# Performance work log

Hardware: AMD Instinct MI355X
Metric: run time of the kernel (lower is better)

## Reference

```python
import jax, jax.numpy as jnp
import numpy as np

N_HEADS, D_MODEL, D_HEAD = 16, 1024, 64
LN_EPS = 1e-5


def setup_inputs() -> dict:
    key = jax.random.key(0)
    ks = jax.random.split(key, 12)
    bs, s = 2, 2048
    hd = N_HEADS * D_HEAD
    sc = 0.02
    return {
        "q": jax.random.normal(ks[0], (bs, s, D_MODEL), jnp.float32),
        "kv": jax.random.normal(ks[1], (bs, s, D_MODEL), jnp.float32),
        "Wq": jax.random.normal(ks[2], (D_MODEL, hd), jnp.float32) * sc,
        "bq": jnp.zeros((hd,), jnp.float32),
        "Wk": jax.random.normal(ks[3], (D_MODEL, hd), jnp.float32) * sc,
        "bk": jnp.zeros((hd,), jnp.float32),
        "Wv": jax.random.normal(ks[4], (D_MODEL, hd), jnp.float32) * sc,
        "bv": jnp.zeros((hd,), jnp.float32),
        "Wo": jax.random.normal(ks[5], (hd, D_MODEL), jnp.float32) * sc,
        "bo": jnp.zeros((D_MODEL,), jnp.float32),
        "gamma": jnp.ones((D_MODEL,), jnp.float32),
        "beta": jnp.zeros((D_MODEL,), jnp.float32),
    }


def _split_heads(x):
    # [b, s, H*D] -> [b, H, s, D]
    b, s, _ = x.shape
    return x.reshape(b, s, N_HEADS, D_HEAD).transpose(0, 2, 1, 3)


def reference(q, kv, Wq, bq, Wk, bk, Wv, bv, Wo, bo, gamma, beta):
    wq = _split_heads(q @ Wq + bq)   # [b,H,Sq,D]
    wk = _split_heads(kv @ Wk + bk)  # [b,H,Sk,D]
    wv = _split_heads(kv @ Wv + bv)  # [b,H,Sk,D]
    scores = jnp.einsum("bhqd,bhkd->bhqk", wq, wk) / jnp.sqrt(
        jnp.asarray(D_HEAD, wq.dtype)
    )
    probs = jax.nn.softmax(scores, axis=-1)  # dropout p=0 -> identity
    attn = jnp.einsum("bhqk,bhkd->bhqd", probs, wv)
    b, _, sq, _ = attn.shape
    attn = attn.transpose(0, 2, 1, 3).reshape(b, sq, N_HEADS * D_HEAD)
    res = q + (attn @ Wo + bo)
    # LayerNorm over last dim
    mu = jnp.mean(res, axis=-1, keepdims=True)
    var = jnp.var(res, axis=-1, keepdims=True)
    return (res - mu) * jax.lax.rsqrt(var + LN_EPS) * gamma + beta
```

## Files before the change

kernel.cpp:

```cpp
#include <hip/hip_runtime.h>
#include <hip/hip_bf16.h>


#define DM 1024
#define SEQ 2048
#define NB 2
#define NH 16
#define DH 64

typedef __attribute__((ext_vector_type(8))) short bf16x8;
typedef __attribute__((ext_vector_type(4))) float f32x4;
typedef __attribute__((ext_vector_type(4))) unsigned int u32x4;

__device__ __forceinline__ float bf2f(short s) {
  unsigned u = ((unsigned)(unsigned short)s) << 16;
  return __builtin_bit_cast(float, u);
}
__device__ __forceinline__ short f2bf(float f) {
  unsigned u = __builtin_bit_cast(unsigned, f);
  u += 0x7fffu + ((u >> 16) & 1u);
  return (short)(u >> 16);
}
__device__ __forceinline__ unsigned cvt_pk_bf16(float lo, float hi) {
  unsigned r;
  asm("v_cvt_pk_bf16_f32 %0, %1, %2" : "=v"(r) : "v"(lo), "v"(hi));
  return r;
}
__device__ __forceinline__ float exp2_fast(float x) {
  float r;
  asm("v_exp_f32 %0, %1" : "=v"(r) : "v"(x));
  return r;
}

#define GLL16(gsrc, ldst)                                                     \
  __builtin_amdgcn_global_load_lds(                                           \
      (const __attribute__((address_space(1))) void*)(gsrc),                  \
      (__attribute__((address_space(3))) void*)(ldst), 16, 0, 0)

#define WAIT_VM(N)                                                            \
  asm volatile("s_waitcnt vmcnt(" #N ")" ::: "memory");                       \
  __builtin_amdgcn_s_barrier();                                               \
  __builtin_amdgcn_sched_barrier(0)

__global__ __launch_bounds__(256) void k_prep(
    const float* __restrict__ q, const float* __restrict__ kv,
    const float* __restrict__ Wq, const float* __restrict__ Wk,
    const float* __restrict__ Wv, const float* __restrict__ Wo,
    short* __restrict__ qb, short* __restrict__ kvb,
    short* __restrict__ Wt_all) {
  const int b = blockIdx.x;
  const int tid = threadIdx.x;
  if (b < 4096) {
    const int i = b * 256 + tid;
    const int half = 524288;
    const float* src = (i < half) ? q : kv;
    short* dst = (i < half) ? qb : kvb;
    const size_t j = (size_t)((i < half) ? i : i - half) * 8;
    const float4 a = *(const float4*)(src + j);
    const float4 c = *(const float4*)(src + j + 4);
    u32x4 pw;
    pw[0] = cvt_pk_bf16(a.x, a.y);
    pw[1] = cvt_pk_bf16(a.z, a.w);
    pw[2] = cvt_pk_bf16(c.x, c.y);
    pw[3] = cvt_pk_bf16(c.z, c.w);
    *(bf16x8*)(dst + j) = __builtin_bit_cast(bf16x8, pw);
  } else {
    const int idx = b - 4096;
    const int z = idx >> 10;
    const int rem = idx & 1023;
    const int n0 = (rem & 31) * 32, k0 = (rem >> 5) * 32;
    const float* src = (z == 0) ? Wq : (z == 1) ? Wk : (z == 2) ? Wv : Wo;
    short* dst = Wt_all + (size_t)z * (DM * DM);
    __shared__ float t[32][33];
    const int tx = tid & 31, ty = tid >> 5;
#pragma unroll
    for (int i = 0; i < 32; i += 8)
      t[ty + i][tx] = src[(size_t)(k0 + ty + i) * DM + n0 + tx];
    __syncthreads();
#pragma unroll
    for (int i = 0; i < 32; i += 8)
      dst[(size_t)(n0 + ty + i) * DM + k0 + tx] = f2bf(t[tx][ty + i]);
  }
}

__device__ __forceinline__ void gemm_body64(short* As, short* Bs,
                                            const short* __restrict__ X,
                                            const short* __restrict__ Wt,
                                            const float* __restrict__ bias,
                                            short* __restrict__ out,
                                            int vt_mode, float cscale,
                                            int bx, int by) {
  const int tid = threadIdx.x;
  const int w = tid >> 6, l = tid & 63;
  const int g = l >> 4, qi = l & 15;
  const int n0 = bx * 128;
  const int m0 = by * 128;
  const int wr = w >> 1, wc = w & 1;

  f32x4 acc[4][4];
#pragma unroll
  for (int m = 0; m < 4; m++)
#pragma unroll
    for (int n = 0; n < 4; n++) acc[m][n] = (f32x4){0.f, 0.f, 0.f, 0.f};

  const int srow = w * 8 + (l >> 3);
  const int scol = ((l & 7) ^ ((l >> 3) & 7)) * 8;
  const short* Ag = X + (size_t)(m0 + srow) * DM + scol;
  const short* Bg = Wt + (size_t)(n0 + srow) * DM + scol;

  for (int k0 = 0; k0 < DM; k0 += 64) {
    __syncthreads();
#pragma unroll
    for (int j = 0; j < 4; j++) {
      GLL16(Ag + (size_t)(j * 32) * DM + k0, As + j * 2048 + w * 512);
      GLL16(Bg + (size_t)(j * 32) * DM + k0, Bs + j * 2048 + w * 512);
    }
    __syncthreads();

#pragma unroll
    for (int kk = 0; kk < 2; kk++) {
      bf16x8 a[4], b[4];
#pragma unroll
      for (int m = 0; m < 4; m++)
        a[m] = *(const bf16x8*)&As[(wr * 64 + m * 16 + qi) * 64 +
                                   (((kk * 4 + g) ^ (qi & 7)) * 8)];
#pragma unroll
      for (int n = 0; n < 4; n++)
        b[n] = *(const bf16x8*)&Bs[(wc * 64 + n * 16 + qi) * 64 +
                                   (((kk * 4 + g) ^ (qi & 7)) * 8)];
#pragma unroll
      for (int m = 0; m < 4; m++)
#pragma unroll
        for (int n = 0; n < 4; n++)
          acc[m][n] = __builtin_amdgcn_mfma_f32_16x16x32_bf16(a[m], b[n],
                                                              acc[m][n], 0, 0, 0);
    }
  }

  const int col0 = n0 + wc * 64;
  const int row0 = m0 + wr * 64;
  float bfv[4];
#pragma unroll
  for (int n = 0; n < 4; n++) bfv[n] = bias[col0 + n * 16 + qi];

  if (!vt_mode) {
#pragma unroll
    for (int m = 0; m < 4; m++) {
#pragma unroll
      for (int n = 0; n < 4; n++) {
        const int col = col0 + n * 16 + qi;
#pragma unroll
        for (int r = 0; r < 4; r++) {
          const int row = row0 + m * 16 + g * 4 + r;
          out[(size_t)row * DM + col] = f2bf((acc[m][n][r] + bfv[n]) * cscale);
        }
      }
    }
  } else {
#pragma unroll
    for (int m = 0; m < 4; m++) {
      const int s_base = row0 + m * 16 + g * 4;
      const int bb = s_base >> 11;
      const int s = s_base & (SEQ - 1);
#pragma unroll
      for (int n = 0; n < 4; n++) {
        const int col = col0 + n * 16 + qi;
        const int h = col >> 6, d = col & 63;
        ushort4 v;
        v.x = (unsigned short)f2bf(acc[m][n][0] + bfv[n]);
        v.y = (unsigned short)f2bf(acc[m][n][1] + bfv[n]);
        v.z = (unsigned short)f2bf(acc[m][n][2] + bfv[n]);
        v.w = (unsigned short)f2bf(acc[m][n][3] + bfv[n]);
        *(ushort4*)&out[(((size_t)bb * NH + h) * DH + d) * SEQ + s] = v;
      }
    }
  }
}

__device__ __forceinline__ void xcd_remap(int& bx, int& by) {
  const int lin2 = blockIdx.x + 8 * blockIdx.y;
  const int xcd = lin2 & 7, jj = lin2 >> 3;
  bx = jj & 7;
  by = xcd * 4 + (jj >> 3);
}

__global__ __launch_bounds__(256) void k_gemm_qkv(
    const short* __restrict__ qb, const short* __restrict__ kvb,
    const short* __restrict__ Wt, const float* __restrict__ bq,
    const float* __restrict__ bk, const float* __restrict__ bv,
    short* __restrict__ qm, short* __restrict__ km, short* __restrict__ vtb) {
  __shared__ short As[8192], Bs[8192];
  const int z = blockIdx.z;
  const short* X = (z == 0) ? qb : kvb;
  const short* W = Wt + (size_t)z * (DM * DM);
  const float* bias = (z == 0) ? bq : (z == 1) ? bk : bv;
  short* out = (z == 0) ? qm : (z == 1) ? km : vtb;
  const float cs = (z == 0) ? 0.18033688011112042f : 1.0f;
  int bx, by;
  xcd_remap(bx, by);
  gemm_body64(As, Bs, X, W, bias, out, z == 2, cs, bx, by);
}

__global__ __launch_bounds__(256) void k_gemm_o(
    const short* __restrict__ attn, const short* __restrict__ Wto,
    const float* __restrict__ bo, short* __restrict__ om) {
  __shared__ short As[8192], Bs[8192];
  int bx, by;
  xcd_remap(bx, by);
  gemm_body64(As, Bs, attn, Wto, bo, om, 0, 1.0f, bx, by);
}

__global__ __launch_bounds__(512) void k_attn(const short* __restrict__ qm,
                                              const short* __restrict__ km,
                                              const short* __restrict__ vt,
                                              short* __restrict__ attn) {
  __shared__ short lds[3][16384];

  const int lin = blockIdx.x;
  const int x = lin & 7, j = lin >> 3;
  const int pair = x + 8 * (j >> 3), qb = j & 7;
  const int h = pair & 15, bb = pair >> 4;
  const int q0 = qb * 256;

  const int tid = threadIdx.x;
  const int w = tid >> 6, l = tid & 63;
  const int g = l >> 4, qi = l & 15;

  const size_t bbS = (size_t)bb * SEQ;
  const size_t vbase = ((size_t)(bb * NH + h)) * DH * SEQ;
  const short* __restrict__ kmh = km + bbS * DM + h * DH;

  const int skey = tid >> 3;
  const int sslot = tid & 7;
  const int kgq = sslot ^ ((skey >> 1) & 7);
  const int vkb = sslot ^ (skey & 7);
  const short* __restrict__ srcK0 = kmh + (size_t)skey * DM + kgq * 8;
  const short* __restrict__ srcV0 = vt + vbase + (size_t)skey * SEQ + vkb * 8;

#define STAGE(buf, kk0)                                                       \
  {                                                                           \
    GLL16(srcK0 + (size_t)(kk0)*DM, &lds[buf][w * 512]);                      \
    GLL16(srcK0 + (size_t)((kk0) + 64) * DM, &lds[buf][4096 + w * 512]);      \
    GLL16(srcV0 + (kk0), &lds[buf][8192 + w * 512]);                          \
    GLL16(srcV0 + (kk0) + 64, &lds[buf][12288 + w * 512]);                    \
  }

  const int rowA = q0 + w * 32 + qi;
  const short* QpA = qm + (bbS + rowA) * DM + h * DH;
  const bf16x8 qA0 = *(const bf16x8*)(QpA + 8 * g);
  const bf16x8 qA1 = *(const bf16x8*)(QpA + 32 + 8 * g);
  const bf16x8 qB0 = *(const bf16x8*)(QpA + 16 * DM + 8 * g);
  const bf16x8 qB1 = *(const bf16x8*)(QpA + 16 * DM + 32 + 8 * g);

  float ssA[4], ssB[4];
#pragma unroll
  for (int i = 0; i < 4; i++) { ssA[i] = 0.f; ssB[i] = 0.f; }
  f32x4 oA[4], oB[4];
#pragma unroll
  for (int f = 0; f < 4; f++) {
    oA[f] = (f32x4){0.f, 0.f, 0.f, 0.f};
    oB[f] = (f32x4){0.f, 0.f, 0.f, 0.f};
  }

  const int xA = (g ^ (qi & 7)) * 8;
  const int xB = ((4 + g) ^ (qi & 7)) * 8;

  auto tile = [&](const short* Ks, const short* Vs) {
    f32x4 sc[2][4];
    __builtin_amdgcn_s_setprio(1);
#pragma unroll
    for (int s = 0; s < 2; s++) {
      const int r0 = (32 * s + 2 * qi) * 64;
      const bf16x8 k00 = *(const bf16x8*)&Ks[r0 + xA];
      const bf16x8 k01 = *(const bf16x8*)&Ks[r0 + xB];
      const bf16x8 k10 = *(const bf16x8*)&Ks[r0 + 64 + xA];
      const bf16x8 k11 = *(const bf16x8*)&Ks[r0 + 64 + xB];
      f32x4 a0 = (f32x4){0.f, 0.f, 0.f, 0.f}, a1 = a0, b0 = a0, b1 = a0;
      a0 = __builtin_amdgcn_mfma_f32_16x16x32_bf16(k00, qA0, a0, 0, 0, 0);
      a0 = __builtin_amdgcn_mfma_f32_16x16x32_bf16(k01, qA1, a0, 0, 0, 0);
      a1 = __builtin_amdgcn_mfma_f32_16x16x32_bf16(k10, qA0, a1, 0, 0, 0);
      a1 = __builtin_amdgcn_mfma_f32_16x16x32_bf16(k11, qA1, a1, 0, 0, 0);
      b0 = __builtin_amdgcn_mfma_f32_16x16x32_bf16(k00, qB0, b0, 0, 0, 0);
      b0 = __builtin_amdgcn_mfma_f32_16x16x32_bf16(k01, qB1, b0, 0, 0, 0);
      b1 = __builtin_amdgcn_mfma_f32_16x16x32_bf16(k10, qB0, b1, 0, 0, 0);
      b1 = __builtin_amdgcn_mfma_f32_16x16x32_bf16(k11, qB1, b1, 0, 0, 0);
      sc[s][0] = a0; sc[s][1] = a1; sc[s][2] = b0; sc[s][3] = b1;
    }
    __builtin_amdgcn_s_setprio(0);

#pragma unroll
    for (int s = 0; s < 2; s++) {
      float eA0[4], eA1[4], eB0[4], eB1[4];
#pragma unroll
      for (int r = 0; r < 4; r++) {
        eA0[r] = exp2_fast(sc[s][0][r]);
        eA1[r] = exp2_fast(sc[s][1][r]);
        eB0[r] = exp2_fast(sc[s][2][r]);
        eB1[r] = exp2_fast(sc[s][3][r]);
      }
#pragma unroll
      for (int r = 0; r < 4; r++) {
        ssA[r] += eA0[r] + eA1[r];
        ssB[r] += eB0[r] + eB1[r];
      }
      u32x4 pwA, pwB;
#pragma unroll
      for (int r = 0; r < 4; r++) {
        pwA[r] = cvt_pk_bf16(eA0[r], eA1[r]);
        pwB[r] = cvt_pk_bf16(eB0[r], eB1[r]);
      }
      const bf16x8 pbA = __builtin_bit_cast(bf16x8, pwA);
      const bf16x8 pbB = __builtin_bit_cast(bf16x8, pwB);

      const int vx = ((4 * s + g) ^ (qi & 7)) * 8;
      __builtin_amdgcn_s_setprio(1);
#pragma unroll
      for (int f = 0; f < 4; f++) {
        const bf16x8 vv = *(const bf16x8*)&Vs[(qi + 16 * f) * 64 + vx];
        oA[f] = __builtin_amdgcn_mfma_f32_16x16x32_bf16(vv, pbA, oA[f], 0, 0, 0);
        oB[f] = __builtin_amdgcn_mfma_f32_16x16x32_bf16(vv, pbB, oB[f], 0, 0, 0);
      }
      __builtin_amdgcn_s_setprio(0);
    }
  };

#define TILE2(B)                                                              \
  tile(&lds[B][0], &lds[B][8192]);                                            \
  tile(&lds[B][4096], &lds[B][12288]);

  STAGE(0, 0);
  STAGE(1, 128);
  for (int kg = 0; kg < 4; ++kg) {
    const int t = kg * 3;
    WAIT_VM(4);
    STAGE(2, (t + 2) * 128);
    TILE2(0)
    WAIT_VM(4);
    STAGE(0, (t + 3) * 128);
    TILE2(1)
    WAIT_VM(4);
    STAGE(1, (t + 4) * 128);
    TILE2(2)
  }
  WAIT_VM(4);
  STAGE(2, 14 * 128);
  TILE2(0)
  WAIT_VM(4);
  STAGE(0, 15 * 128);
  TILE2(1)
  WAIT_VM(4);
  TILE2(2)
  WAIT_VM(0);
  TILE2(0)

  float sa = (ssA[0] + ssA[1]) + (ssA[2] + ssA[3]);
  sa += __shfl_xor(sa, 16);
  sa += __shfl_xor(sa, 32);
  const float invA = 1.f / sa;
  float sb = (ssB[0] + ssB[1]) + (ssB[2] + ssB[3]);
  sb += __shfl_xor(sb, 16);
  sb += __shfl_xor(sb, 32);
  const float invB = 1.f / sb;

  short* OpA = attn + (bbS + rowA) * DM + h * DH;
#pragma unroll
  for (int f = 0; f < 4; f++) {
    ushort4 v;
    v.x = (unsigned short)f2bf(oA[f][0] * invA);
    v.y = (unsigned short)f2bf(oA[f][1] * invA);
    v.z = (unsigned short)f2bf(oA[f][2] * invA);
    v.w = (unsigned short)f2bf(oA[f][3] * invA);
    *(ushort4*)(OpA + f * 16 + g * 4) = v;
    ushort4 u;
    u.x = (unsigned short)f2bf(oB[f][0] * invB);
    u.y = (unsigned short)f2bf(oB[f][1] * invB);
    u.z = (unsigned short)f2bf(oB[f][2] * invB);
    u.w = (unsigned short)f2bf(oB[f][3] * invB);
    *(ushort4*)(OpA + 16 * DM + f * 16 + g * 4) = u;
  }
#undef STAGE
#undef TILE2
}

__global__ __launch_bounds__(256) void k_ln(const float* __restrict__ q,
                                            const short* __restrict__ om,
                                            const float* __restrict__ gamma,
                                            const float* __restrict__ beta,
                                            float* __restrict__ out) {
  const int row = blockIdx.x;
  const int t = threadIdx.x;
  const int w = t >> 6, l = t & 63;
  const size_t base = (size_t)row * DM + t * 4;
  const float4 qv = *(const float4*)(q + base);
  const ushort4 ov = *(const ushort4*)(om + base);
  float v[4];
  v[0] = qv.x + bf2f((short)ov.x);
  v[1] = qv.y + bf2f((short)ov.y);
  v[2] = qv.z + bf2f((short)ov.z);
  v[3] = qv.w + bf2f((short)ov.w);
  float s = v[0] + v[1] + v[2] + v[3];
  float s2 = v[0] * v[0] + v[1] * v[1] + v[2] * v[2] + v[3] * v[3];
#pragma unroll
  for (int off = 32; off >= 1; off >>= 1) {
    s += __shfl_xor(s, off);
    s2 += __shfl_xor(s2, off);
  }
  __shared__ float ps[4], ps2[4];
  if (l == 0) {
    ps[w] = s;
    ps2[w] = s2;
  }
  __syncthreads();
  const float St = ps[0] + ps[1] + ps[2] + ps[3];
  const float S2t = ps2[0] + ps2[1] + ps2[2] + ps2[3];
  const float mu = St * (1.f / 1024.f);
  float var = S2t * (1.f / 1024.f) - mu * mu;
  const float rstd = rsqrtf(var + 1e-5f);
  const float4 gv = *(const float4*)(gamma + t * 4);
  const float4 bv = *(const float4*)(beta + t * 4);
  float4 ovv;
  ovv.x = (v[0] - mu) * rstd * gv.x + bv.x;
  ovv.y = (v[1] - mu) * rstd * gv.y + bv.y;
  ovv.z = (v[2] - mu) * rstd * gv.z + bv.z;
  ovv.w = (v[3] - mu) * rstd * gv.w + bv.w;
  *(float4*)(out + base) = ovv;
}

extern "C" void kernel_launch(void* const* d_in, const int* in_sizes, int n_in,
                              void* d_out, int out_size, void* d_ws, size_t ws_size,
                              hipStream_t stream) {
  const float* q = (const float*)d_in[0];
  const float* kv = (const float*)d_in[1];
  const float* Wq = (const float*)d_in[2];
  const float* bq = (const float*)d_in[3];
  const float* Wk = (const float*)d_in[4];
  const float* bk = (const float*)d_in[5];
  const float* Wv = (const float*)d_in[6];
  const float* bv = (const float*)d_in[7];
  const float* Wo = (const float*)d_in[8];
  const float* bo = (const float*)d_in[9];
  const float* gamma = (const float*)d_in[10];
  const float* beta = (const float*)d_in[11];

  short* ws = (short*)d_ws;
  short* Wt = ws;
  short* qb16 = ws + 4u * 1048576u;
  short* kvb16 = qb16 + 4194304u;
  short* qm = kvb16 + 4194304u;
  short* km = qm + 4194304u;
  short* vtb = km + 4194304u;
  short* attnb = qb16;
  short* om = kvb16;

  hipLaunchKernelGGL(k_prep, dim3(8192), dim3(256), 0, stream,
                     q, kv, Wq, Wk, Wv, Wo, qb16, kvb16, Wt);
  hipLaunchKernelGGL(k_gemm_qkv, dim3(8, 32, 3), dim3(256), 0, stream,
                     qb16, kvb16, Wt, bq, bk, bv, qm, km, vtb);
  hipLaunchKernelGGL(k_attn, dim3(256), dim3(512), 0, stream,
                     qm, km, vtb, attnb);
  hipLaunchKernelGGL(k_gemm_o, dim3(8, 32, 1), dim3(256), 0, stream,
                     attnb, Wt + 3u * 1048576u, bo, om);
  hipLaunchKernelGGL(k_ln, dim3(4096), dim3(256), 0, stream,
                     q, om, gamma, beta, (float*)d_out);
}
```

Baseline: 117.8 us.

## Fuse K and V projections into one GEMM sharing the kv activation tile

Splits the combined QKV GEMM launch into a Q GEMM and a fused K/V GEMM. The fused kernel loads each kv activation tile into LDS once and multiplies it against both Wk and Wv tiles, keeping two accumulator sets. This halves activation traffic for the K/V projections, but doubles accumulator registers (lowering occupancy), uses more LDS, and adds a second serial launch with fewer blocks per launch.

```diff
diff --git a/kernel.cpp b/kernel.cpp
--- a/kernel.cpp
+++ b/kernel.cpp
@@ -184,21 +184,117 @@
   by = xcd * 4 + (jj >> 3);
 }
 
-__global__ __launch_bounds__(256) void k_gemm_qkv(
-    const short* __restrict__ qb, const short* __restrict__ kvb,
-    const short* __restrict__ Wt, const float* __restrict__ bq,
-    const float* __restrict__ bk, const float* __restrict__ bv,
-    short* __restrict__ qm, short* __restrict__ km, short* __restrict__ vtb) {
+__global__ __launch_bounds__(256) void k_gemm_q(
+    const short* __restrict__ qb, const short* __restrict__ Wtq,
+    const float* __restrict__ bq, short* __restrict__ qm) {
   __shared__ short As[8192], Bs[8192];
-  const int z = blockIdx.z;
-  const short* X = (z == 0) ? qb : kvb;
-  const short* W = Wt + (size_t)z * (DM * DM);
-  const float* bias = (z == 0) ? bq : (z == 1) ? bk : bv;
-  short* out = (z == 0) ? qm : (z == 1) ? km : vtb;
-  const float cs = (z == 0) ? 0.18033688011112042f : 1.0f;
   int bx, by;
   xcd_remap(bx, by);
-  gemm_body64(As, Bs, X, W, bias, out, z == 2, cs, bx, by);
+  gemm_body64(As, Bs, qb, Wtq, bq, qm, 0, 0.18033688011112042f, bx, by);
+}
+
+__global__ __launch_bounds__(256) void k_gemm_kv(
+    const short* __restrict__ kvb, const short* __restrict__ Wtk,
+    const short* __restrict__ Wtv, const float* __restrict__ bk,
+    const float* __restrict__ bv, short* __restrict__ km,
+    short* __restrict__ vtb) {
+  __shared__ short As[8192], Bks[8192], Bvs[8192];
+  const int tid = threadIdx.x;
+  const int w = tid >> 6, l = tid & 63;
+  const int g = l >> 4, qi = l & 15;
+  int bx, by;
+  xcd_remap(bx, by);
+  const int n0 = bx * 128;
+  const int m0 = by * 128;
+  const int wr = w >> 1, wc = w & 1;
+
+  f32x4 accK[4][4], accV[4][4];
+#pragma unroll
+  for (int m = 0; m < 4; m++)
+#pragma unroll
+    for (int n = 0; n < 4; n++) {
+      accK[m][n] = (f32x4){0.f, 0.f, 0.f, 0.f};
+      accV[m][n] = (f32x4){0.f, 0.f, 0.f, 0.f};
+    }
+
+  const int srow = w * 8 + (l >> 3);
+  const int scol = ((l & 7) ^ ((l >> 3) & 7)) * 8;
+  const short* Ag = kvb + (size_t)(m0 + srow) * DM + scol;
+  const short* Bkg = Wtk + (size_t)(n0 + srow) * DM + scol;
+  const short* Bvg = Wtv + (size_t)(n0 + srow) * DM + scol;
+
+  for (int k0 = 0; k0 < DM; k0 += 64) {
+    __syncthreads();
+#pragma unroll
+    for (int j = 0; j < 4; j++) {
+      GLL16(Ag + (size_t)(j * 32) * DM + k0, As + j * 2048 + w * 512);
+      GLL16(Bkg + (size_t)(j * 32) * DM + k0, Bks + j * 2048 + w * 512);
+      GLL16(Bvg + (size_t)(j * 32) * DM + k0, Bvs + j * 2048 + w * 512);
+    }
+    __syncthreads();
+
+#pragma unroll
+    for (int kk = 0; kk < 2; kk++) {
+      const int xo0 = (((kk * 4 + g) ^ (qi & 7)) * 8);
+      bf16x8 a[4], bk_[4], bv_[4];
+#pragma unroll
+      for (int m = 0; m < 4; m++)
+        a[m] = *(const bf16x8*)&As[(wr * 64 + m * 16 + qi) * 64 + xo0];
+#pragma unroll
+      for (int n = 0; n < 4; n++) {
+        bk_[n] = *(const bf16x8*)&Bks[(wc * 64 + n * 16 + qi) * 64 + xo0];
+        bv_[n] = *(const bf16x8*)&Bvs[(wc * 64 + n * 16 + qi) * 64 + xo0];
+      }
+#pragma unroll
+      for (int m = 0; m < 4; m++)
+#pragma unroll
+        for (int n = 0; n < 4; n++) {
+          accK[m][n] = __builtin_amdgcn_mfma_f32_16x16x32_bf16(a[m], bk_[n],
+                                                               accK[m][n], 0, 0, 0);
+          accV[m][n] = __builtin_amdgcn_mfma_f32_16x16x32_bf16(a[m], bv_[n],
+                                                               accV[m][n], 0, 0, 0);
+        }
+    }
+  }
+
+  const int col0 = n0 + wc * 64;
+  const int row0 = m0 + wr * 64;
+  float bkv[4], bvv[4];
+#pragma unroll
+  for (int n = 0; n < 4; n++) {
+    bkv[n] = bk[col0 + n * 16 + qi];
+    bvv[n] = bv[col0 + n * 16 + qi];
+  }
+
+#pragma unroll
+  for (int m = 0; m < 4; m++) {
+#pragma unroll
+    for (int n = 0; n < 4; n++) {
+      const int col = col0 + n * 16 + qi;
+#pragma unroll
+      for (int r = 0; r < 4; r++) {
+        const int row = row0 + m * 16 + g * 4 + r;
+        km[(size_t)row * DM + col] = f2bf(accK[m][n][r] + bkv[n]);
+      }
+    }
+  }
+#pragma unroll
+  for (int m = 0; m < 4; m++) {
+    const int s_base = row0 + m * 16 + g * 4;
+    const int bb = s_base >> 11;
+    const int s = s_base & (SEQ - 1);
+#pragma unroll
+    for (int n = 0; n < 4; n++) {
+      const int col = col0 + n * 16 + qi;
+      const int h = col >> 6, d = col & 63;
+      ushort4 v;
+      v.x = (unsigned short)f2bf(accV[m][n][0] + bvv[n]);
+      v.y = (unsigned short)f2bf(accV[m][n][1] + bvv[n]);
+      v.z = (unsigned short)f2bf(accV[m][n][2] + bvv[n]);
+      v.w = (unsigned short)f2bf(accV[m][n][3] + bvv[n]);
+      *(ushort4*)&vtb[(((size_t)bb * NH + h) * DH + d) * SEQ + s] = v;
+    }
+  }
 }
 
 __global__ __launch_bounds__(256) void k_gemm_o(
@@ -454,8 +550,11 @@
 
   hipLaunchKernelGGL(k_prep, dim3(8192), dim3(256), 0, stream,
                      q, kv, Wq, Wk, Wv, Wo, qb16, kvb16, Wt);
-  hipLaunchKernelGGL(k_gemm_qkv, dim3(8, 32, 3), dim3(256), 0, stream,
-                     qb16, kvb16, Wt, bq, bk, bv, qm, km, vtb);
+  hipLaunchKernelGGL(k_gemm_q, dim3(8, 32), dim3(256), 0, stream,
+                     qb16, Wt, bq, qm);
+  hipLaunchKernelGGL(k_gemm_kv, dim3(8, 32), dim3(256), 0, stream,
+                     kvb16, Wt + 1u * 1048576u, Wt + 2u * 1048576u,
+                     bk, bv, km, vtb);
   hipLaunchKernelGGL(k_attn, dim3(256), dim3(512), 0, stream,
                      qm, km, vtb, attnb);
   hipLaunchKernelGGL(k_gemm_o, dim3(8, 32, 1), dim3(256), 0, stream,
```

Result: slower. 128.5 us (+9.1%).
